# Kernel optimization log

Measured on AMD Instinct MI355X. Metric: run time of the kernel, lower is better.

Reference implementation:

```python
import jax, jax.numpy as jnp
import numpy as np

N_NODES = 100000


def _deg_isqrt(idx, n):
    # clamped-to-1 degree, then ^-0.5 (DGL GraphConv norm='both')
    deg = jax.ops.segment_sum(jnp.ones(idx.shape, jnp.float32), idx, num_segments=n)
    return jnp.power(jnp.maximum(deg, 1.0), -0.5)


def _graph_conv(feat, W, b, src, dst, out_isqrt, in_isqrt, n):
    # norm='both': scale by src out-degree^-1/2, mult-first (in>out), spmm, scale by dst in-degree^-1/2
    h = (feat * out_isqrt[:, None]) @ W                      # [N, out]
    h = jax.ops.segment_sum(h[src], dst, num_segments=n)     # gather/scatter over edges
    return h * in_isqrt[:, None] + b


def setup_inputs() -> dict:
    key = jax.random.key(0)
    ks = jax.random.split(key, 10)
    in_dim, h1, h2 = 512, 64, 32
    n, e = N_NODES, 800000
    features = jax.random.normal(ks[0], (n, in_dim), jnp.float32)
    src = jax.random.randint(ks[1], (e,), 0, n)
    dst = jax.random.randint(ks[2], (e,), 0, n)
    noise = jax.random.normal(ks[3], (n, h2), jnp.float32)
    s1 = 1.0 / np.sqrt(in_dim)
    s2 = 1.0 / np.sqrt(h1)
    W1 = jax.random.uniform(ks[4], (in_dim, h1), jnp.float32, -s1, s1)
    b1 = jnp.zeros((h1,), jnp.float32)
    W2 = jax.random.uniform(ks[5], (h1, h2), jnp.float32, -s2, s2)
    b2 = jnp.zeros((h2,), jnp.float32)
    W3 = jax.random.uniform(ks[6], (h1, h2), jnp.float32, -s2, s2)
    b3 = jnp.zeros((h2,), jnp.float32)
    return {"features": features, "src": src, "dst": dst, "noise": noise,
            "W1": W1, "b1": b1, "W2": W2, "b2": b2, "W3": W3, "b3": b3}


def reference(features, src, dst, noise, W1, b1, W2, b2, W3, b3):
    n = features.shape[0]
    out_isqrt = _deg_isqrt(src, n)
    in_isqrt = _deg_isqrt(dst, n)
    h = jax.nn.relu(_graph_conv(features, W1, b1, src, dst, out_isqrt, in_isqrt, n))
    mean = _graph_conv(h, W2, b2, src, dst, out_isqrt, in_isqrt, n)
    log_std = _graph_conv(h, W3, b3, src, dst, out_isqrt, in_isqrt, n)
    z = mean + noise * jnp.exp(log_std)
    return z, mean, log_std
```

## Files before the change

kernel.cpp:

```cpp
#include <hip/hip_runtime.h>
#include <hip/hip_bf16.h>


typedef __attribute__((ext_vector_type(8))) short short8;
typedef __attribute__((ext_vector_type(4))) float f32x4;
typedef unsigned short ushort_t;

static __device__ inline short f2bf(float f)
{
    union { __hip_bfloat16 h; short s; } u;
    u.h = __float2bfloat16(f);
    return u.s;
}

static __device__ inline float bf2f(ushort_t u)
{
    union { float f; unsigned v; } w;
    w.v = ((unsigned)u) << 16;
    return w.f;
}

static __device__ inline short8 cvt8(float4 lo, float4 hi)
{
    short8 r;
    r[0] = f2bf(lo.x); r[1] = f2bf(lo.y); r[2] = f2bf(lo.z); r[3] = f2bf(lo.w);
    r[4] = f2bf(hi.x); r[5] = f2bf(hi.y); r[6] = f2bf(hi.z); r[7] = f2bf(hi.w);
    return r;
}

__global__ __launch_bounds__(256) void k_setup(
    const float* __restrict__ W1, const float* __restrict__ W2,
    const float* __restrict__ W3, short* __restrict__ w1f,
    float* __restrict__ wc, int4* __restrict__ zp, int z4)
{
    int gid = blockIdx.x * 256 + threadIdx.x;
    if (gid < z4) zp[gid] = make_int4(0, 0, 0, 0);
    if (gid < 64 * 64) {
        int k = gid >> 6, c = gid & 63;
        wc[gid] = (c < 32) ? W2[k * 32 + c] : W3[k * 32 + (c - 32)];
    }
    if (gid < 512 * 64) {
        int k = gid >> 6, c = gid & 63;
        int kt = k >> 5, kk = k & 31, nt = c >> 4, lr = c & 15;
        int kg = kk >> 3, j = kk & 7;
        int l = kg * 16 + lr;
        w1f[(kt * 4 + nt) * 512 + l * 8 + j] = f2bf(W1[gid]);
    }
}

__global__ __launch_bounds__(256) void k_deg_int(
    const int* __restrict__ src, const int* __restrict__ dst,
    int* __restrict__ degS, int* __restrict__ degD, int e)
{
    int gid = blockIdx.x * 256 + threadIdx.x;
    if (gid >= e) return;
    atomicAdd(&degS[src[gid]], 1);
    atomicAdd(&degD[dst[gid]], 1);
}

__global__ __launch_bounds__(256) void k_scan_block_sums(
    const int* __restrict__ deg, int* __restrict__ partials, int n)
{
    __shared__ int red[256];
    int gid = blockIdx.x * 256 + threadIdx.x;
    red[threadIdx.x] = (gid < n) ? deg[gid] : 0;
    __syncthreads();
    for (int s = 128; s > 0; s >>= 1) {
        if (threadIdx.x < s) red[threadIdx.x] += red[threadIdx.x + s];
        __syncthreads();
    }
    if (threadIdx.x == 0) partials[blockIdx.x] = red[0];
}

__global__ __launch_bounds__(512) void k_scan_partials(
    int* __restrict__ partials, int nb)
{
    __shared__ int s[512];
    int t = threadIdx.x;
    s[t] = (t < nb) ? partials[t] : 0;
    __syncthreads();
    for (int d = 1; d < 512; d <<= 1) {
        int v = (t >= d) ? s[t - d] : 0;
        __syncthreads();
        s[t] += v;
        __syncthreads();
    }
    if (t < nb) partials[t] = (t == 0) ? 0 : s[t - 1];
}

__global__ __launch_bounds__(256) void k_scan_final(
    const int* __restrict__ degD, const int* __restrict__ degS,
    const int* __restrict__ partials,
    int* __restrict__ row_ptr, int* __restrict__ cursor,
    float* __restrict__ isq_out, float* __restrict__ isq_in, int n)
{
    __shared__ int s[256];
    int t = threadIdx.x;
    int gid = blockIdx.x * 256 + t;
    int v = (gid < n) ? degD[gid] : 0;
    s[t] = v;
    __syncthreads();
    for (int d = 1; d < 256; d <<= 1) {
        int u = (t >= d) ? s[t - d] : 0;
        __syncthreads();
        s[t] += u;
        __syncthreads();
    }
    int start = partials[blockIdx.x] + s[t] - v;
    if (gid < n) {
        row_ptr[gid] = start;
        cursor[gid]  = start;
        isq_in[gid]  = 1.0f / sqrtf((float)max(v, 1));
        isq_out[gid] = 1.0f / sqrtf((float)max(degS[gid], 1));
    }
    if (gid == n - 1) row_ptr[n] = start + v;
}

__global__ __launch_bounds__(256) void k_scatter(
    const int* __restrict__ src, const int* __restrict__ dst,
    int* __restrict__ cursor, int* __restrict__ edge_src, int e)
{
    int gid = blockIdx.x * 256 + threadIdx.x;
    if (gid >= e) return;
    int pos = atomicAdd(&cursor[dst[gid]], 1);
    edge_src[pos] = src[gid];
}

__global__ __launch_bounds__(256) void k_gemm1_mfma(
    const float* __restrict__ X, const short* __restrict__ w1f,
    const float* __restrict__ scale, ushort_t* __restrict__ Y, int n)
{
    const int tid  = threadIdx.x;
    const int l    = tid & 63;
    const int wv   = tid >> 6;
    const int row0 = (blockIdx.x * 4 + wv) * 16;
    const int lr   = l & 15;
    const int kg   = l >> 4;

    int ra = row0 + lr;  if (ra >= n) ra = n - 1;
    const float* pa = X + (size_t)ra * 512 + kg * 8;
    const short* pb = w1f + l * 8;

    f32x4 acc[4];
#pragma unroll
    for (int j = 0; j < 4; ++j) acc[j] = (f32x4){0.f, 0.f, 0.f, 0.f};

    float4 alo0 = *(const float4*)(pa);
    float4 ahi0 = *(const float4*)(pa + 4);
    float4 alo1 = *(const float4*)(pa + 32);
    float4 ahi1 = *(const float4*)(pa + 36);
    short8 b0 = *(const short8*)(pb);
    short8 b1 = *(const short8*)(pb + 512);
    short8 b2 = *(const short8*)(pb + 1024);
    short8 b3 = *(const short8*)(pb + 1536);

#pragma unroll
    for (int kt = 0; kt < 16; ++kt) {
        short8 ca = (kt & 1) ? cvt8(alo1, ahi1) : cvt8(alo0, ahi0);
        if (kt + 2 < 16) {
            const float* q = pa + (kt + 2) * 32;
            if (kt & 1) { alo1 = *(const float4*)(q); ahi1 = *(const float4*)(q + 4); }
            else        { alo0 = *(const float4*)(q); ahi0 = *(const float4*)(q + 4); }
        }
        short8 cb0 = b0, cb1 = b1, cb2 = b2, cb3 = b3;
        if (kt + 1 < 16) {
            const short* q = pb + (size_t)(kt + 1) * 2048;
            b0 = *(const short8*)(q);
            b1 = *(const short8*)(q + 512);
            b2 = *(const short8*)(q + 1024);
            b3 = *(const short8*)(q + 1536);
        }
        acc[0] = __builtin_amdgcn_mfma_f32_16x16x32_bf16(ca, cb0, acc[0], 0, 0, 0);
        acc[1] = __builtin_amdgcn_mfma_f32_16x16x32_bf16(ca, cb1, acc[1], 0, 0, 0);
        acc[2] = __builtin_amdgcn_mfma_f32_16x16x32_bf16(ca, cb2, acc[2], 0, 0, 0);
        acc[3] = __builtin_amdgcn_mfma_f32_16x16x32_bf16(ca, cb3, acc[3], 0, 0, 0);
    }

#pragma unroll
    for (int m = 0; m < 4; ++m) {
        int row = row0 + kg * 4 + m;
        if (row < n) {
            float s = scale[row];
#pragma unroll
            for (int nt = 0; nt < 4; ++nt)
                Y[(size_t)row * 64 + nt * 16 + lr] =
                    (ushort_t)f2bf(acc[nt][m] * s);
        }
    }
}

__global__ __launch_bounds__(256) void k_gather_h(
    const int* __restrict__ row_ptr, const int* __restrict__ edge_src,
    const ushort_t* __restrict__ x, const float* __restrict__ isq_in,
    const float* __restrict__ isq_out, const float* __restrict__ b1,
    float* __restrict__ h, int n)
{
    int col  = threadIdx.x & 63;
    int node = __builtin_amdgcn_readfirstlane(blockIdx.x * 4 + (threadIdx.x >> 6));
    if (node >= n) return;
    float si = isq_in[node];
    float so = isq_out[node];
    float bb = b1[col];
    int j = row_ptr[node], jend = row_ptr[node + 1];
    float a0 = 0.f, a1 = 0.f, a2 = 0.f, a3 = 0.f;
    float a4 = 0.f, a5 = 0.f, a6 = 0.f, a7 = 0.f;
    for (; j + 7 < jend; j += 8) {
        int e0 = edge_src[j],     e1 = edge_src[j + 1];
        int e2 = edge_src[j + 2], e3 = edge_src[j + 3];
        int e4 = edge_src[j + 4], e5 = edge_src[j + 5];
        int e6 = edge_src[j + 6], e7 = edge_src[j + 7];
        a0 += bf2f(x[(size_t)e0 * 64 + col]);
        a1 += bf2f(x[(size_t)e1 * 64 + col]);
        a2 += bf2f(x[(size_t)e2 * 64 + col]);
        a3 += bf2f(x[(size_t)e3 * 64 + col]);
        a4 += bf2f(x[(size_t)e4 * 64 + col]);
        a5 += bf2f(x[(size_t)e5 * 64 + col]);
        a6 += bf2f(x[(size_t)e6 * 64 + col]);
        a7 += bf2f(x[(size_t)e7 * 64 + col]);
    }
    for (; j + 1 < jend; j += 2) {
        int e0 = edge_src[j], e1 = edge_src[j + 1];
        a0 += bf2f(x[(size_t)e0 * 64 + col]);
        a1 += bf2f(x[(size_t)e1 * 64 + col]);
    }
    if (j < jend) a2 += bf2f(x[(size_t)edge_src[j] * 64 + col]);
    float acc = ((a0 + a1) + (a2 + a3)) + ((a4 + a5) + (a6 + a7));
    h[(size_t)node * 64 + col] = fmaxf(acc * si + bb, 0.f) * so;
}

__global__ __launch_bounds__(256) void k_gemm2(
    const float* __restrict__ X, const float* __restrict__ W,
    ushort_t* __restrict__ Y, int n)
{
    __shared__ float sx[64][68];
    __shared__ float sw[64][64];
    const int tid  = threadIdx.x;
    const int colp = tid & 31;
    const int rg   = tid >> 5;
    const int row0 = blockIdx.x * 64;

    float2 acc[8];
#pragma unroll
    for (int i = 0; i < 8; ++i) acc[i] = make_float2(0.f, 0.f);

#pragma unroll
    for (int p = 0; p < 4; ++p) {
        int u = p * 256 + tid;
        int r = u >> 4, c4 = (u & 15) * 4;
        int row = row0 + r;
        float4 v = make_float4(0.f, 0.f, 0.f, 0.f);
        if (row < n) v = *(const float4*)&X[(size_t)row * 64 + c4];
        *(float4*)&sx[r][c4] = v;
        *(float4*)&sw[r][c4] = *(const float4*)&W[u * 4];
    }
    __syncthreads();

#pragma unroll 4
    for (int k4 = 0; k4 < 64; k4 += 4) {
        float2 w0 = *(const float2*)&sw[k4 + 0][colp * 2];
        float2 w1 = *(const float2*)&sw[k4 + 1][colp * 2];
        float2 w2 = *(const float2*)&sw[k4 + 2][colp * 2];
        float2 w3 = *(const float2*)&sw[k4 + 3][colp * 2];
#pragma unroll
        for (int i = 0; i < 8; ++i) {
            float4 f = *(const float4*)&sx[rg * 8 + i][k4];
            acc[i].x += f.x * w0.x + f.y * w1.x + f.z * w2.x + f.w * w3.x;
            acc[i].y += f.x * w0.y + f.y * w1.y + f.z * w2.y + f.w * w3.y;
        }
    }

#pragma unroll
    for (int i = 0; i < 8; ++i) {
        int row = row0 + rg * 8 + i;
        if (row < n) {
            unsigned lo = (unsigned)(unsigned short)f2bf(acc[i].x);
            unsigned hi = (unsigned)(unsigned short)f2bf(acc[i].y);
            ((unsigned*)Y)[(size_t)row * 32 + colp] = (hi << 16) | lo;
        }
    }
}

__global__ __launch_bounds__(256) void k_gather_final(
    const int* __restrict__ row_ptr, const int* __restrict__ edge_src,
    const ushort_t* __restrict__ t23, const float* __restrict__ isq_in,
    const float* __restrict__ b2, const float* __restrict__ b3,
    const float* __restrict__ noise, float* __restrict__ out, int n)
{
    int lane = threadIdx.x & 63;
    int node = __builtin_amdgcn_readfirstlane(blockIdx.x * 4 + (threadIdx.x >> 6));
    if (node >= n) return;
    float si   = isq_in[node];
    float bias = (lane < 32) ? b2[lane] : b3[lane - 32];
    int total  = n * 32;
    int base   = node * 32 + (lane & 31);
    float nz   = (lane < 32) ? noise[base] : 0.f;
    int j = row_ptr[node], jend = row_ptr[node + 1];
    float a0 = 0.f, a1 = 0.f, a2 = 0.f, a3 = 0.f;
    float a4 = 0.f, a5 = 0.f, a6 = 0.f, a7 = 0.f;
    for (; j + 7 < jend; j += 8) {
        int e0 = edge_src[j],     e1 = edge_src[j + 1];
        int e2 = edge_src[j + 2], e3 = edge_src[j + 3];
        int e4 = edge_src[j + 4], e5 = edge_src[j + 5];
        int e6 = edge_src[j + 6], e7 = edge_src[j + 7];
        a0 += bf2f(t23[(size_t)e0 * 64 + lane]);
        a1 += bf2f(t23[(size_t)e1 * 64 + lane]);
        a2 += bf2f(t23[(size_t)e2 * 64 + lane]);
        a3 += bf2f(t23[(size_t)e3 * 64 + lane]);
        a4 += bf2f(t23[(size_t)e4 * 64 + lane]);
        a5 += bf2f(t23[(size_t)e5 * 64 + lane]);
        a6 += bf2f(t23[(size_t)e6 * 64 + lane]);
        a7 += bf2f(t23[(size_t)e7 * 64 + lane]);
    }
    for (; j + 1 < jend; j += 2) {
        int e0 = edge_src[j], e1 = edge_src[j + 1];
        a0 += bf2f(t23[(size_t)e0 * 64 + lane]);
        a1 += bf2f(t23[(size_t)e1 * 64 + lane]);
    }
    if (j < jend) a2 += bf2f(t23[(size_t)edge_src[j] * 64 + lane]);
    float acc = ((a0 + a1) + (a2 + a3)) + ((a4 + a5) + (a6 + a7));
    float v  = acc * si + bias;
    float lv = __shfl(v, lane | 32, 64);
    if (lane < 32) {
        float z = v + nz * expf(lv);
        out[base]         = z;
        out[total + base] = v;
    } else {
        out[2 * total + base] = v;
    }
}

extern "C" void kernel_launch(void* const* d_in, const int* in_sizes, int n_in,
                              void* d_out, int out_size, void* d_ws, size_t ws_size,
                              hipStream_t stream)
{
    const float* feat  = (const float*)d_in[0];
    const int*   src   = (const int*)d_in[1];
    const int*   dst   = (const int*)d_in[2];
    const float* noise = (const float*)d_in[3];
    const float* W1    = (const float*)d_in[4];
    const float* b1    = (const float*)d_in[5];
    const float* W2    = (const float*)d_in[6];
    const float* b2    = (const float*)d_in[7];
    const float* W3    = (const float*)d_in[8];
    const float* b3    = (const float*)d_in[9];

    const int n = in_sizes[0] / 512;
    const int e = in_sizes[1];

    float* ws      = (float*)d_ws;
    float* isq_out = ws;
    float* isq_in  = ws + n;
    float* bufA    = ws + 2 * (size_t)n;
    float* bufB    = bufA + 64 * (size_t)n;
    float* wc      = bufB + 64 * (size_t)n;
    short* w1f     = (short*)(wc + 64 * 64);
    int*   ip      = (int*)(w1f + 512 * 64);
    int* row_ptr   = ip;
    int* cursor    = ip + (n + 1);
    int* partials  = cursor + n;
    int* edge_src  = partials + 512;
    int* degS = (int*)bufA;
    int* degD = degS + n;
    float* out = (float*)d_out;

    const int nb = (n + 255) / 256;
    const int z4 = (2 * n) / 4;

    k_setup<<<(z4 + 255) / 256, 256, 0, stream>>>(
        W1, W2, W3, w1f, wc, (int4*)degS, z4);

    k_deg_int<<<(e + 255) / 256, 256, 0, stream>>>(src, dst, degS, degD, e);

    k_scan_block_sums<<<nb, 256, 0, stream>>>(degD, partials, n);
    k_scan_partials<<<1, 512, 0, stream>>>(partials, nb);
    k_scan_final<<<nb, 256, 0, stream>>>(
        degD, degS, partials, row_ptr, cursor, isq_out, isq_in, n);
    k_scatter<<<(e + 255) / 256, 256, 0, stream>>>(src, dst, cursor, edge_src, e);

    k_gemm1_mfma<<<(n + 63) / 64, 256, 0, stream>>>(
        feat, w1f, isq_out, (ushort_t*)bufA, n);

    k_gather_h<<<(n + 3) / 4, 256, 0, stream>>>(
        row_ptr, edge_src, (const ushort_t*)bufA, isq_in, isq_out, b1, bufB, n);

    k_gemm2<<<(n + 63) / 64, 256, 0, stream>>>(bufB, wc, (ushort_t*)bufA, n);

    k_gather_final<<<(n + 3) / 4, 256, 0, stream>>>(
        row_ptr, edge_src, (const ushort_t*)bufA, isq_in, b2, b3, noise, out, n);
}
```

Before: 266.4 us.

## Fuse layer-1 gather with second GEMM and deepen GEMM1 prefetch

Merges the layer-1 neighbour aggregation and the 64x64 projection into one kernel. Each wave aggregates a node row, stages it in LDS, and multiplies it by the combined W2/W3 weights held in shared memory. This removes the fp32 hidden-feature round trip through global memory and one kernel launch. Separately, GEMM1 now prefetches A four k-steps ahead and B two steps ahead to hide more load latency. The cost is more register pressure, and each block has to reload 16KB of weights into LDS for only 16 nodes.

```diff
diff --git a/kernel.cpp b/kernel.cpp
--- a/kernel.cpp
+++ b/kernel.cpp
@@ -145,30 +145,38 @@
 #pragma unroll
     for (int j = 0; j < 4; ++j) acc[j] = (f32x4){0.f, 0.f, 0.f, 0.f};
 
-    float4 alo0 = *(const float4*)(pa);
-    float4 ahi0 = *(const float4*)(pa + 4);
-    float4 alo1 = *(const float4*)(pa + 32);
-    float4 ahi1 = *(const float4*)(pa + 36);
-    short8 b0 = *(const short8*)(pb);
-    short8 b1 = *(const short8*)(pb + 512);
-    short8 b2 = *(const short8*)(pb + 1024);
-    short8 b3 = *(const short8*)(pb + 1536);
+    float4 alo[4], ahi[4];
+#pragma unroll
+    for (int s = 0; s < 4; ++s) {
+        alo[s] = *(const float4*)(pa + s * 32);
+        ahi[s] = *(const float4*)(pa + s * 32 + 4);
+    }
+    short8 bst[2][4];
+#pragma unroll
+    for (int s = 0; s < 2; ++s) {
+        const short* q = pb + (size_t)s * 2048;
+        bst[s][0] = *(const short8*)(q);
+        bst[s][1] = *(const short8*)(q + 512);
+        bst[s][2] = *(const short8*)(q + 1024);
+        bst[s][3] = *(const short8*)(q + 1536);
+    }
 
 #pragma unroll
     for (int kt = 0; kt < 16; ++kt) {
-        short8 ca = (kt & 1) ? cvt8(alo1, ahi1) : cvt8(alo0, ahi0);
+        short8 ca = cvt8(alo[kt & 3], ahi[kt & 3]);
+        if (kt + 4 < 16) {
+            const float* q = pa + (kt + 4) * 32;
+            alo[kt & 3] = *(const float4*)(q);
+            ahi[kt & 3] = *(const float4*)(q + 4);
+        }
+        short8 cb0 = bst[kt & 1][0], cb1 = bst[kt & 1][1];
+        short8 cb2 = bst[kt & 1][2], cb3 = bst[kt & 1][3];
         if (kt + 2 < 16) {
-            const float* q = pa + (kt + 2) * 32;
-            if (kt & 1) { alo1 = *(const float4*)(q); ahi1 = *(const float4*)(q + 4); }
-            else        { alo0 = *(const float4*)(q); ahi0 = *(const float4*)(q + 4); }
-        }
-        short8 cb0 = b0, cb1 = b1, cb2 = b2, cb3 = b3;
-        if (kt + 1 < 16) {
-            const short* q = pb + (size_t)(kt + 1) * 2048;
-            b0 = *(const short8*)(q);
-            b1 = *(const short8*)(q + 512);
-            b2 = *(const short8*)(q + 1024);
-            b3 = *(const short8*)(q + 1536);
+            const short* q = pb + (size_t)(kt + 2) * 2048;
+            bst[kt & 1][0] = *(const short8*)(q);
+            bst[kt & 1][1] = *(const short8*)(q + 512);
+            bst[kt & 1][2] = *(const short8*)(q + 1024);
+            bst[kt & 1][3] = *(const short8*)(q + 1536);
         }
         acc[0] = __builtin_amdgcn_mfma_f32_16x16x32_bf16(ca, cb0, acc[0], 0, 0, 0);
         acc[1] = __builtin_amdgcn_mfma_f32_16x16x32_bf16(ca, cb1, acc[1], 0, 0, 0);
@@ -189,94 +197,73 @@
     }
 }
 
-__global__ __launch_bounds__(256) void k_gather_h(
+__global__ __launch_bounds__(256) void k_gather_gemm2(
     const int* __restrict__ row_ptr, const int* __restrict__ edge_src,
     const ushort_t* __restrict__ x, const float* __restrict__ isq_in,
     const float* __restrict__ isq_out, const float* __restrict__ b1,
-    float* __restrict__ h, int n)
-{
-    int col  = threadIdx.x & 63;
-    int node = __builtin_amdgcn_readfirstlane(blockIdx.x * 4 + (threadIdx.x >> 6));
-    if (node >= n) return;
-    float si = isq_in[node];
-    float so = isq_out[node];
-    float bb = b1[col];
-    int j = row_ptr[node], jend = row_ptr[node + 1];
-    float a0 = 0.f, a1 = 0.f, a2 = 0.f, a3 = 0.f;
-    float a4 = 0.f, a5 = 0.f, a6 = 0.f, a7 = 0.f;
-    for (; j + 7 < jend; j += 8) {
-        int e0 = edge_src[j],     e1 = edge_src[j + 1];
-        int e2 = edge_src[j + 2], e3 = edge_src[j + 3];
-        int e4 = edge_src[j + 4], e5 = edge_src[j + 5];
-        int e6 = edge_src[j + 6], e7 = edge_src[j + 7];
-        a0 += bf2f(x[(size_t)e0 * 64 + col]);
-        a1 += bf2f(x[(size_t)e1 * 64 + col]);
-        a2 += bf2f(x[(size_t)e2 * 64 + col]);
-        a3 += bf2f(x[(size_t)e3 * 64 + col]);
-        a4 += bf2f(x[(size_t)e4 * 64 + col]);
-        a5 += bf2f(x[(size_t)e5 * 64 + col]);
-        a6 += bf2f(x[(size_t)e6 * 64 + col]);
-        a7 += bf2f(x[(size_t)e7 * 64 + col]);
-    }
-    for (; j + 1 < jend; j += 2) {
-        int e0 = edge_src[j], e1 = edge_src[j + 1];
-        a0 += bf2f(x[(size_t)e0 * 64 + col]);
-        a1 += bf2f(x[(size_t)e1 * 64 + col]);
-    }
-    if (j < jend) a2 += bf2f(x[(size_t)edge_src[j] * 64 + col]);
-    float acc = ((a0 + a1) + (a2 + a3)) + ((a4 + a5) + (a6 + a7));
-    h[(size_t)node * 64 + col] = fmaxf(acc * si + bb, 0.f) * so;
-}
-
-__global__ __launch_bounds__(256) void k_gemm2(
-    const float* __restrict__ X, const float* __restrict__ W,
-    ushort_t* __restrict__ Y, int n)
-{
-    __shared__ float sx[64][68];
-    __shared__ float sw[64][64];
-    const int tid  = threadIdx.x;
-    const int colp = tid & 31;
-    const int rg   = tid >> 5;
-    const int row0 = blockIdx.x * 64;
-
-    float2 acc[8];
-#pragma unroll
-    for (int i = 0; i < 8; ++i) acc[i] = make_float2(0.f, 0.f);
+    const float* __restrict__ wc, ushort_t* __restrict__ t23, int n)
+{
+    __shared__ float swc[64 * 64];
+    __shared__ float sh[4][64];
+    const int tid = threadIdx.x;
+    const int col = tid & 63;
+    const int wv  = tid >> 6;
 
 #pragma unroll
     for (int p = 0; p < 4; ++p) {
         int u = p * 256 + tid;
-        int r = u >> 4, c4 = (u & 15) * 4;
-        int row = row0 + r;
-        float4 v = make_float4(0.f, 0.f, 0.f, 0.f);
-        if (row < n) v = *(const float4*)&X[(size_t)row * 64 + c4];
-        *(float4*)&sx[r][c4] = v;
-        *(float4*)&sw[r][c4] = *(const float4*)&W[u * 4];
+        *(float4*)&swc[u * 4] = *(const float4*)&wc[u * 4];
     }
     __syncthreads();
 
-#pragma unroll 4
-    for (int k4 = 0; k4 < 64; k4 += 4) {
-        float2 w0 = *(const float2*)&sw[k4 + 0][colp * 2];
-        float2 w1 = *(const float2*)&sw[k4 + 1][colp * 2];
-        float2 w2 = *(const float2*)&sw[k4 + 2][colp * 2];
-        float2 w3 = *(const float2*)&sw[k4 + 3][colp * 2];
-#pragma unroll
-        for (int i = 0; i < 8; ++i) {
-            float4 f = *(const float4*)&sx[rg * 8 + i][k4];
-            acc[i].x += f.x * w0.x + f.y * w1.x + f.z * w2.x + f.w * w3.x;
-            acc[i].y += f.x * w0.y + f.y * w1.y + f.z * w2.y + f.w * w3.y;
-        }
-    }
-
-#pragma unroll
-    for (int i = 0; i < 8; ++i) {
-        int row = row0 + rg * 8 + i;
-        if (row < n) {
-            unsigned lo = (unsigned)(unsigned short)f2bf(acc[i].x);
-            unsigned hi = (unsigned)(unsigned short)f2bf(acc[i].y);
-            ((unsigned*)Y)[(size_t)row * 32 + colp] = (hi << 16) | lo;
-        }
+    const float bb = b1[col];
+
+#pragma unroll 1
+    for (int i = 0; i < 4; ++i) {
+        int node = blockIdx.x * 16 + wv * 4 + i;
+        if (node >= n) break;
+        float si = isq_in[node];
+        float so = isq_out[node];
+        int j = row_ptr[node], jend = row_ptr[node + 1];
+        float a0 = 0.f, a1 = 0.f, a2 = 0.f, a3 = 0.f;
+        float a4 = 0.f, a5 = 0.f, a6 = 0.f, a7 = 0.f;
+        for (; j + 7 < jend; j += 8) {
+            int e0 = edge_src[j],     e1 = edge_src[j + 1];
+            int e2 = edge_src[j + 2], e3 = edge_src[j + 3];
+            int e4 = edge_src[j + 4], e5 = edge_src[j + 5];
+            int e6 = edge_src[j + 6], e7 = edge_src[j + 7];
+            a0 += bf2f(x[(size_t)e0 * 64 + col]);
+            a1 += bf2f(x[(size_t)e1 * 64 + col]);
+            a2 += bf2f(x[(size_t)e2 * 64 + col]);
+            a3 += bf2f(x[(size_t)e3 * 64 + col]);
+            a4 += bf2f(x[(size_t)e4 * 64 + col]);
+            a5 += bf2f(x[(size_t)e5 * 64 + col]);
+            a6 += bf2f(x[(size_t)e6 * 64 + col]);
+            a7 += bf2f(x[(size_t)e7 * 64 + col]);
+        }
+        for (; j + 1 < jend; j += 2) {
+            int e0 = edge_src[j], e1 = edge_src[j + 1];
+            a0 += bf2f(x[(size_t)e0 * 64 + col]);
+            a1 += bf2f(x[(size_t)e1 * 64 + col]);
+        }
+        if (j < jend) a2 += bf2f(x[(size_t)edge_src[j] * 64 + col]);
+        float acc = ((a0 + a1) + (a2 + a3)) + ((a4 + a5) + (a6 + a7));
+        float hval = fmaxf(acc * si + bb, 0.f) * so;
+
+        sh[wv][col] = hval;
+        asm volatile("s_waitcnt lgkmcnt(0)" ::: "memory");
+        __builtin_amdgcn_sched_barrier(0);
+
+        float t = 0.f;
+#pragma unroll
+        for (int k4 = 0; k4 < 64; k4 += 4) {
+            float4 hb = *(const float4*)&sh[wv][k4];
+            t += hb.x * swc[(k4 + 0) * 64 + col]
+               + hb.y * swc[(k4 + 1) * 64 + col]
+               + hb.z * swc[(k4 + 2) * 64 + col]
+               + hb.w * swc[(k4 + 3) * 64 + col];
+        }
+        t23[(size_t)node * 64 + col] = (ushort_t)f2bf(t);
     }
 }
 
@@ -380,11 +367,10 @@
     k_gemm1_mfma<<<(n + 63) / 64, 256, 0, stream>>>(
         feat, w1f, isq_out, (ushort_t*)bufA, n);
 
-    k_gather_h<<<(n + 3) / 4, 256, 0, stream>>>(
-        row_ptr, edge_src, (const ushort_t*)bufA, isq_in, isq_out, b1, bufB, n);
-
-    k_gemm2<<<(n + 63) / 64, 256, 0, stream>>>(bufB, wc, (ushort_t*)bufA, n);
+    k_gather_gemm2<<<(n + 15) / 16, 256, 0, stream>>>(
+        row_ptr, edge_src, (const ushort_t*)bufA, isq_in, isq_out, b1,
+        wc, (ushort_t*)bufB, n);
 
     k_gather_final<<<(n + 3) / 4, 256, 0, stream>>>(
-        row_ptr, edge_src, (const ushort_t*)bufA, isq_in, b2, b3, noise, out, n);
-}
+        row_ptr, edge_src, (const ushort_t*)bufB, isq_in, b2, b3, noise, out, n);
+}
```

Result: no change. 264.7 us, median of 2 (-0.7%).
